# Optimization experiments

Measured on AMD Instinct MI355X. Metric: run time of the kernel, lower is better.

Reference implementation:

```python
import jax, jax.numpy as jnp
import numpy as np

NUM_FEATURES = 40960
EMB_DIM = 2048


def setup_inputs() -> dict:
    key = jax.random.key(0)
    ks = jax.random.split(key, 8)
    B, L = 4096, 32
    white = jax.random.randint(ks[0], (B, L), 0, NUM_FEATURES, dtype=jnp.int64)
    black = jax.random.randint(ks[1], (B, L), 0, NUM_FEATURES, dtype=jnp.int64)
    stm = jax.random.randint(ks[2], (B,), 0, 2, dtype=jnp.int64)
    emb_table = jax.random.normal(ks[3], (NUM_FEATURES, EMB_DIM), dtype=jnp.float32) * 0.02
    W1 = jax.random.normal(ks[4], (128, 2 * EMB_DIM), dtype=jnp.float32) * 0.02
    b1 = jax.random.normal(ks[5], (128,), dtype=jnp.float32) * 0.02
    W2 = jax.random.normal(ks[6], (1, 128), dtype=jnp.float32) * 0.02
    b2 = jax.random.normal(ks[7], (1,), dtype=jnp.float32) * 0.02
    return {"white": white, "black": black, "stm": stm,
            "emb_table": emb_table, "W1": W1, "b1": b1, "W2": W2, "b2": b2}


def _encode(emb_table, idx):
    # idx: [B, L] padded with 0; embedding gather then mask out padding (index 0)
    emb = emb_table[idx]                         # [B, L, D]
    mask = (idx != 0)[..., None].astype(emb.dtype)
    return (emb * mask).sum(axis=1)              # [B, D]


def reference(white, black, stm, emb_table, W1, b1, W2, b2):
    w = _encode(emb_table, white)                # [B, D]
    b = _encode(emb_table, black)                # [B, D]
    wb = jnp.concatenate([w, b], axis=1)         # [B, 2D]
    bw = jnp.concatenate([b, w], axis=1)
    x = jnp.where((stm == 1)[:, None], wb, bw)
    h = jax.nn.relu(x @ W1.T + b1)               # [B, 128]
    return h @ W2.T + b2                         # [B, 1]
```

## Files before the change

### kernel.cpp

```cpp
#include <hip/hip_runtime.h>
#include <cstddef>

typedef __bf16 bf16x8 __attribute__((ext_vector_type(8)));
typedef float  floatx4 __attribute__((ext_vector_type(4)));

static __device__ __forceinline__ unsigned short f2bf(float f) {
    unsigned int u = __float_as_uint(f);
    u = u + 0x7fff + ((u >> 16) & 1);
    return (unsigned short)(u >> 16);
}
static __device__ __forceinline__ float bflo(unsigned int u) {
    return __uint_as_float(u << 16);
}
static __device__ __forceinline__ float bfhi(unsigned int u) {
    return __uint_as_float(u & 0xffff0000u);
}

__global__ __launch_bounds__(256) void nnue_convw1(
    const float* __restrict__ W1, unsigned short* __restrict__ W1b)
{
    const int i = (blockIdx.x * 256 + threadIdx.x) * 4;
    const float4 v = *reinterpret_cast<const float4*>(W1 + i);
    ushort4 o;
    o.x = f2bf(v.x); o.y = f2bf(v.y); o.z = f2bf(v.z); o.w = f2bf(v.w);
    *reinterpret_cast<ushort4*>(W1b + i) = o;
}

#define ALDS 72
__global__ __launch_bounds__(256) void nnue_pgemm(
    const float* __restrict__ emb, const unsigned short* __restrict__ w1b,
    unsigned short* __restrict__ P)
{
    __shared__ unsigned short As[128 * ALDS];
    __shared__ unsigned short Bs[128 * 64];

    const int t    = threadIdx.x;
    const int wid  = t >> 6;
    const int lane = t & 63;
    const int quad = lane >> 4;
    const int l16  = lane & 15;
    const int wm   = wid >> 1;
    const int wn   = wid & 1;
    const int fbase = (blockIdx.x >> 1) * 128;
    const int nblk  = blockIdx.x & 1;

    const int bsrc_shorts = (((lane & 7) ^ (lane >> 3)) << 3);
    const int brow        = lane >> 3;

    floatx4 acc[4][4];
#pragma unroll
    for (int i = 0; i < 4; ++i)
#pragma unroll
        for (int j = 0; j < 4; ++j) acc[i][j] = (floatx4){0.f, 0.f, 0.f, 0.f};

    for (int kc = 0; kc < 2048; kc += 64) {
        __syncthreads();
#pragma unroll
        for (int i = 0; i < 4; ++i) {
            const int c = wid * 4 + i;
            const int r = c * 8 + brow;
            const unsigned short* g = w1b + (size_t)r * 4096 + nblk * 2048
                                    + kc + bsrc_shorts;
            auto* dst = (__attribute__((address_space(3))) unsigned int*)(Bs + c * 512);
            __builtin_amdgcn_global_load_lds(
                (const __attribute__((address_space(1))) unsigned int*)g,
                dst, 16, 0, 0);
        }
#pragma unroll
        for (int i = 0; i < 8; ++i) {
            const int cch = t + i * 256;
            const int row = cch >> 4, cc = cch & 15;
            const float4 v = *reinterpret_cast<const float4*>(
                emb + (size_t)(fbase + row) * 2048 + kc + cc * 4);
            ushort4 o;
            o.x = f2bf(v.x); o.y = f2bf(v.y); o.z = f2bf(v.z); o.w = f2bf(v.w);
            *reinterpret_cast<ushort4*>(As + row * ALDS + cc * 4) = o;
        }
        __syncthreads();
#pragma unroll
        for (int kk = 0; kk < 64; kk += 32) {
            bf16x8 a[4], b[4];
#pragma unroll
            for (int mi = 0; mi < 4; ++mi)
                a[mi] = *reinterpret_cast<const bf16x8*>(
                    As + (wm * 64 + mi * 16 + l16) * ALDS + kk + quad * 8);
#pragma unroll
            for (int ni = 0; ni < 4; ++ni) {
                const int r  = wn * 64 + ni * 16 + l16;
                const int cb = (kk * 2 + quad * 16) ^ ((r & 7) << 4);
                b[ni] = *reinterpret_cast<const bf16x8*>(
                    reinterpret_cast<const char*>(Bs) + r * 128 + cb);
            }
#pragma unroll
            for (int mi = 0; mi < 4; ++mi)
#pragma unroll
                for (int ni = 0; ni < 4; ++ni)
                    acc[mi][ni] = __builtin_amdgcn_mfma_f32_16x16x32_bf16(
                        a[mi], b[ni], acc[mi][ni], 0, 0, 0);
        }
    }

#pragma unroll
    for (int mi = 0; mi < 4; ++mi)
#pragma unroll
        for (int ni = 0; ni < 4; ++ni) {
            const int n = nblk * 128 + wn * 64 + ni * 16 + l16;
#pragma unroll
            for (int r = 0; r < 4; ++r) {
                const int f = fbase + wm * 64 + mi * 16 + quad * 4 + r;
                P[(size_t)f * 256 + n] = f2bf(acc[mi][ni][r]);
            }
        }
}

__global__ __launch_bounds__(256) void nnue_out(
    const int* __restrict__ white, const int* __restrict__ black,
    const int* __restrict__ stm, const unsigned short* __restrict__ P,
    const float* __restrict__ b1, const float* __restrict__ W2,
    const float* __restrict__ b2, float* __restrict__ out)
{
    __shared__ int sW[128], sB[128];
    const int t = threadIdx.x;
    const int bbase = blockIdx.x * 4;
    if (t < 128) sW[t] = white[bbase * 32 + t];
    else         sB[t - 128] = black[bbase * 32 + (t - 128)];
    __syncthreads();

    const int w = t >> 6, lane = t & 63;
    const int b = bbase + w;
    const int offw = (stm[b] != 0) ? 0 : 128;
    const int offb = 128 - offw;
    const int n2 = lane * 2;

    float h0 = 0.f, h1 = 0.f;
#pragma unroll
    for (int i = 0; i < 32; ++i) {
        const int iw = sW[w * 32 + i];
        const unsigned int uw = *reinterpret_cast<const unsigned int*>(
            P + (size_t)iw * 256 + offw + n2);
        const float mw = (iw != 0) ? 1.f : 0.f;
        h0 += bflo(uw) * mw;
        h1 += bfhi(uw) * mw;

        const int ib = sB[w * 32 + i];
        const unsigned int ub = *reinterpret_cast<const unsigned int*>(
            P + (size_t)ib * 256 + offb + n2);
        const float mb = (ib != 0) ? 1.f : 0.f;
        h0 += bflo(ub) * mb;
        h1 += bfhi(ub) * mb;
    }

    h0 += b1[n2];     h1 += b1[n2 + 1];
    h0 = (h0 > 0.f) ? h0 : 0.f;
    h1 = (h1 > 0.f) ? h1 : 0.f;
    float s = h0 * W2[n2] + h1 * W2[n2 + 1];
#pragma unroll
    for (int m = 1; m < 64; m <<= 1) s += __shfl_xor(s, m, 64);
    if (lane == 0) out[b] = s + b2[0];
}

extern "C" void kernel_launch(void* const* d_in, const int* in_sizes, int n_in,
                              void* d_out, int out_size, void* d_ws, size_t ws_size,
                              hipStream_t stream)
{
    const int*   white = (const int*)d_in[0];
    const int*   black = (const int*)d_in[1];
    const int*   stm   = (const int*)d_in[2];
    const float* emb   = (const float*)d_in[3];
    const float* W1    = (const float*)d_in[4];
    const float* b1    = (const float*)d_in[5];
    const float* W2    = (const float*)d_in[6];
    const float* b2    = (const float*)d_in[7];
    float* out = (float*)d_out;

    unsigned short* w1buf = (unsigned short*)d_ws;
    unsigned short* pbuf  = w1buf + (size_t)128 * 4096;

    nnue_convw1<<<512, 256, 0, stream>>>(W1, w1buf);
    nnue_pgemm<<<640, 256, 0, stream>>>(emb, w1buf, pbuf);
    nnue_out<<<1024, 256, 0, stream>>>(white, black, stm, pbuf, b1, W2, b2, out);
}
```

Before: 524.5 us.

## Load each embedding tile once per block via async LDS copy, convert in registers

The precompute GEMM now covers all 256 output columns per block with 512 threads, so each embedding row tile is read from HBM once instead of twice. The fp32 embedding tile is streamed straight into swizzled LDS with global_load_lds and converted to bf16 when fragments are read, replacing the synchronous load-convert-store path. The output kernel splits white and black gathers across separate waves and combines them through shared memory, doubling the number of blocks. This costs more LDS (fp32 A tile) and repeated conversions per wave, and lowers occupancy per block.

```diff
diff --git a/kernel.cpp b/kernel.cpp
--- a/kernel.cpp
+++ b/kernel.cpp
@@ -26,26 +26,26 @@
     *reinterpret_cast<ushort4*>(W1b + i) = o;
 }
 
-#define ALDS 72
-__global__ __launch_bounds__(256) void nnue_pgemm(
+__global__ __launch_bounds__(512) void nnue_pgemm(
     const float* __restrict__ emb, const unsigned short* __restrict__ w1b,
     unsigned short* __restrict__ P)
 {
-    __shared__ unsigned short As[128 * ALDS];
-    __shared__ unsigned short Bs[128 * 64];
+    __shared__ float          Asf[128 * 64];
+    __shared__ unsigned short Bs[256 * 64];
 
     const int t    = threadIdx.x;
     const int wid  = t >> 6;
     const int lane = t & 63;
     const int quad = lane >> 4;
     const int l16  = lane & 15;
-    const int wm   = wid >> 1;
-    const int wn   = wid & 1;
-    const int fbase = (blockIdx.x >> 1) * 128;
-    const int nblk  = blockIdx.x & 1;
+    const int wm   = wid >> 2;
+    const int wn   = wid & 3;
+    const int fbase = blockIdx.x * 128;
 
-    const int bsrc_shorts = (((lane & 7) ^ (lane >> 3)) << 3);
-    const int brow        = lane >> 3;
+    const int bRow       = lane >> 3;
+    const int bSrcShorts = (((lane & 7) ^ bRow) << 3);
+    const int aRowIn     = lane >> 4;
+    const int aUnit      = lane & 15;
 
     floatx4 acc[4][4];
 #pragma unroll
@@ -57,33 +57,42 @@
         __syncthreads();
 #pragma unroll
         for (int i = 0; i < 4; ++i) {
-            const int c = wid * 4 + i;
-            const int r = c * 8 + brow;
-            const unsigned short* g = w1b + (size_t)r * 4096 + nblk * 2048
-                                    + kc + bsrc_shorts;
-            auto* dst = (__attribute__((address_space(3))) unsigned int*)(Bs + c * 512);
+            const int cA = wid * 4 + i;
+            const int rA = cA * 4 + aRowIn;
+            const int uA = aUnit ^ (rA & 7);
+            const float* gA = emb + (size_t)(fbase + rA) * 2048 + kc + uA * 4;
+            auto* dA = (__attribute__((address_space(3))) unsigned int*)(Asf + cA * 256);
             __builtin_amdgcn_global_load_lds(
-                (const __attribute__((address_space(1))) unsigned int*)g,
-                dst, 16, 0, 0);
-        }
-#pragma unroll
-        for (int i = 0; i < 8; ++i) {
-            const int cch = t + i * 256;
-            const int row = cch >> 4, cc = cch & 15;
-            const float4 v = *reinterpret_cast<const float4*>(
-                emb + (size_t)(fbase + row) * 2048 + kc + cc * 4);
-            ushort4 o;
-            o.x = f2bf(v.x); o.y = f2bf(v.y); o.z = f2bf(v.z); o.w = f2bf(v.w);
-            *reinterpret_cast<ushort4*>(As + row * ALDS + cc * 4) = o;
+                (const __attribute__((address_space(1))) unsigned int*)gA, dA, 16, 0, 0);
+
+            const int cB = wid * 4 + i;
+            const int rB = cB * 8 + bRow;
+            const unsigned short* gB = w1b + (size_t)(rB & 127) * 4096
+                                     + (rB >> 7) * 2048 + kc + bSrcShorts;
+            auto* dB = (__attribute__((address_space(3))) unsigned int*)(Bs + cB * 512);
+            __builtin_amdgcn_global_load_lds(
+                (const __attribute__((address_space(1))) unsigned int*)gB, dB, 16, 0, 0);
         }
         __syncthreads();
 #pragma unroll
         for (int kk = 0; kk < 64; kk += 32) {
             bf16x8 a[4], b[4];
 #pragma unroll
-            for (int mi = 0; mi < 4; ++mi)
-                a[mi] = *reinterpret_cast<const bf16x8*>(
-                    As + (wm * 64 + mi * 16 + l16) * ALDS + kk + quad * 8);
+            for (int mi = 0; mi < 4; ++mi) {
+                const int row = wm * 64 + mi * 16 + l16;
+                const int cb0 = kk * 4 + quad * 32;
+                const char* base = reinterpret_cast<const char*>(Asf) + row * 256;
+                const float4 lo = *reinterpret_cast<const float4*>(
+                    base + ((cb0)      ^ ((row & 7) << 4)));
+                const float4 hi = *reinterpret_cast<const float4*>(
+                    base + ((cb0 + 16) ^ ((row & 7) << 4)));
+                bf16x8 av;
+                av[0] = (__bf16)lo.x; av[1] = (__bf16)lo.y;
+                av[2] = (__bf16)lo.z; av[3] = (__bf16)lo.w;
+                av[4] = (__bf16)hi.x; av[5] = (__bf16)hi.y;
+                av[6] = (__bf16)hi.z; av[7] = (__bf16)hi.w;
+                a[mi] = av;
+            }
 #pragma unroll
             for (int ni = 0; ni < 4; ++ni) {
                 const int r  = wn * 64 + ni * 16 + l16;
@@ -104,7 +113,7 @@
     for (int mi = 0; mi < 4; ++mi)
 #pragma unroll
         for (int ni = 0; ni < 4; ++ni) {
-            const int n = nblk * 128 + wn * 64 + ni * 16 + l16;
+            const int n = wn * 64 + ni * 16 + l16;
 #pragma unroll
             for (int r = 0; r < 4; ++r) {
                 const int f = fbase + wm * 64 + mi * 16 + quad * 4 + r;
@@ -119,44 +128,48 @@
     const float* __restrict__ b1, const float* __restrict__ W2,
     const float* __restrict__ b2, float* __restrict__ out)
 {
-    __shared__ int sW[128], sB[128];
+    __shared__ int sW[64], sB[64];
+    __shared__ float red[4][64][2];
     const int t = threadIdx.x;
-    const int bbase = blockIdx.x * 4;
-    if (t < 128) sW[t] = white[bbase * 32 + t];
-    else         sB[t - 128] = black[bbase * 32 + (t - 128)];
+    const int bbase = blockIdx.x * 2;
+    if (t < 64)       sW[t] = white[bbase * 32 + t];
+    else if (t < 128) sB[t - 64] = black[bbase * 32 + (t - 64)];
     __syncthreads();
 
     const int w = t >> 6, lane = t & 63;
-    const int b = bbase + w;
-    const int offw = (stm[b] != 0) ? 0 : 128;
-    const int offb = 128 - offw;
+    const int pair = w >> 1;
+    const int b = bbase + pair;
+    const bool isW = ((w & 1) == 0);
+    const int stm_b = stm[b];
+    const int off = isW ? ((stm_b != 0) ? 0 : 128)
+                        : ((stm_b != 0) ? 128 : 0);
+    const int* lst = isW ? (sW + pair * 32) : (sB + pair * 32);
     const int n2 = lane * 2;
 
     float h0 = 0.f, h1 = 0.f;
 #pragma unroll
     for (int i = 0; i < 32; ++i) {
-        const int iw = sW[w * 32 + i];
-        const unsigned int uw = *reinterpret_cast<const unsigned int*>(
-            P + (size_t)iw * 256 + offw + n2);
-        const float mw = (iw != 0) ? 1.f : 0.f;
-        h0 += bflo(uw) * mw;
-        h1 += bfhi(uw) * mw;
+        const int idx = lst[i];
+        const unsigned int u = *reinterpret_cast<const unsigned int*>(
+            P + (size_t)idx * 256 + off + n2);
+        const float m = (idx != 0) ? 1.f : 0.f;
+        h0 += bflo(u) * m;
+        h1 += bfhi(u) * m;
+    }
+    red[w][lane][0] = h0;
+    red[w][lane][1] = h1;
+    __syncthreads();
 
-        const int ib = sB[w * 32 + i];
-        const unsigned int ub = *reinterpret_cast<const unsigned int*>(
-            P + (size_t)ib * 256 + offb + n2);
-        const float mb = (ib != 0) ? 1.f : 0.f;
-        h0 += bflo(ub) * mb;
-        h1 += bfhi(ub) * mb;
+    if (isW) {
+        float H0 = red[w][lane][0] + red[w + 1][lane][0] + b1[n2];
+        float H1 = red[w][lane][1] + red[w + 1][lane][1] + b1[n2 + 1];
+        H0 = (H0 > 0.f) ? H0 : 0.f;
+        H1 = (H1 > 0.f) ? H1 : 0.f;
+        float s = H0 * W2[n2] + H1 * W2[n2 + 1];
+#pragma unroll
+        for (int m = 1; m < 64; m <<= 1) s += __shfl_xor(s, m, 64);
+        if (lane == 0) out[b] = s + b2[0];
     }
-
-    h0 += b1[n2];     h1 += b1[n2 + 1];
-    h0 = (h0 > 0.f) ? h0 : 0.f;
-    h1 = (h1 > 0.f) ? h1 : 0.f;
-    float s = h0 * W2[n2] + h1 * W2[n2 + 1];
-#pragma unroll
-    for (int m = 1; m < 64; m <<= 1) s += __shfl_xor(s, m, 64);
-    if (lane == 0) out[b] = s + b2[0];
 }
 
 extern "C" void kernel_launch(void* const* d_in, const int* in_sizes, int n_in,
@@ -177,6 +190,6 @@
     unsigned short* pbuf  = w1buf + (size_t)128 * 4096;
 
     nnue_convw1<<<512, 256, 0, stream>>>(W1, w1buf);
-    nnue_pgemm<<<640, 256, 0, stream>>>(emb, w1buf, pbuf);
-    nnue_out<<<1024, 256, 0, stream>>>(white, black, stm, pbuf, b1, W2, b2, out);
+    nnue_pgemm<<<320, 512, 0, stream>>>(emb, w1buf, pbuf);
+    nnue_out<<<2048, 256, 0, stream>>>(white, black, stm, pbuf, b1, W2, b2, out);
 }
```

Result: slower. 549.6 us (+4.8%).
